# Kernel optimization log

Hardware: AMD Instinct MI355X
Metric: run time of the kernel (lower is better)

## Reference

```python
import jax, jax.numpy as jnp
import numpy as np

B, T, D = 2, 2048, 2048
NH, NKV = 16, 4
HD = D // NH  # 128
BASE, TSL = 10000.0, 1024


def rotary_tables(T, hd, base=BASE, tsl=TSL):
    # Matches Rotary.forward with rd == hd (rd=0 in __init__ -> full head dim).
    ar = jnp.arange(0, hd, 2, dtype=jnp.float32) / hd
    if T <= tsl:
        inv = 1.0 / (base ** ar)
    else:
        # NTK-style rescale; note right-assoc exponent in original torch code:
        # 1/(base * (T/tsl) ** ((rd/(rd-2)) ** ar))
        inv = 1.0 / (base * jnp.power(T / tsl, jnp.power(hd / (hd - 2.0), ar)))
    f = jnp.outer(jnp.arange(T, dtype=jnp.float32), inv)  # [T, hd//2]
    cos = jnp.cos(f)[None, :, None, :]  # [1,T,1,hd//2]
    sin = jnp.sin(f)[None, :, None, :]
    return cos, sin


def apply_rope(x, cos, sin):
    # full-dim rope: split halves, rotate
    h = x.shape[-1] // 2
    x1, x2 = x[..., :h], x[..., h:]
    return jnp.concatenate((x1 * cos + x2 * sin, -x1 * sin + x2 * cos), axis=-1)


def rms_norm(x):
    eps = jnp.finfo(x.dtype).eps
    return x * jax.lax.rsqrt(jnp.mean(x * x, axis=-1, keepdims=True) + eps)


def setup_inputs() -> dict:
    key = jax.random.key(0)
    k0, k1, k2, k3, k4 = jax.random.split(key, 5)
    s = 0.02
    return {
        "x": jax.random.normal(k0, (B, T, D), jnp.float32),
        "qw": jax.random.normal(k1, (NH * HD, D), jnp.float32) * s,
        "kw": jax.random.normal(k2, (NKV * HD, D), jnp.float32) * s,
        "vw": jax.random.normal(k3, (NKV * HD, D), jnp.float32) * s,
        "ow": jax.random.normal(k4, (D, D), jnp.float32) * s,
        "qg": jnp.ones((NH,), jnp.float32),
    }


def reference(x, qw, kw, vw, ow, qg):
    Bx, Tx, Dx = x.shape
    q = (x @ qw.T).reshape(Bx, Tx, NH, HD)
    k = (x @ kw.T).reshape(Bx, Tx, NKV, HD)
    v = (x @ vw.T).reshape(Bx, Tx, NKV, HD)
    q = rms_norm(q)
    k = rms_norm(k)
    cos, sin = rotary_tables(Tx, HD)
    q = apply_rope(q, cos, sin) * qg[None, None, :, None]
    k = apply_rope(k, cos, sin)
    # GQA: repeat kv heads
    r = NH // NKV
    k = jnp.repeat(k, r, axis=2)  # [B,T,NH,HD]
    v = jnp.repeat(v, r, axis=2)
    scale = 1.0 / jnp.sqrt(jnp.asarray(HD, q.dtype))
    scores = jnp.einsum("bqhd,bkhd->bhqk", q, k) * scale  # [B,NH,T,T]
    causal = jnp.tril(jnp.ones((Tx, Tx), dtype=bool))
    scores = jnp.where(causal[None, None, :, :], scores, jnp.asarray(-jnp.inf, scores.dtype))
    attn = jax.nn.softmax(scores, axis=-1)
    y = jnp.einsum("bhqk,bkhd->bqhd", attn, v)  # [B,T,NH,HD]
    return y.reshape(Bx, Tx, Dx) @ ow.T
```

## Files before the change

### kernel.cpp

```cpp
#include <hip/hip_runtime.h>
#include <hip/hip_bf16.h>
#include <stdint.h>


typedef __attribute__((ext_vector_type(8))) short short8;
typedef __attribute__((ext_vector_type(4))) float f32x4;
typedef __attribute__((ext_vector_type(16))) float f32x16;

#define GLOAD16(gp, lp) \
  __builtin_amdgcn_global_load_lds((const __attribute__((address_space(1))) void*)(gp), \
                                   (__attribute__((address_space(3))) void*)(lp), 16, 0, 0)

#define BAR() do { asm volatile("" ::: "memory"); __builtin_amdgcn_s_barrier(); asm volatile("" ::: "memory"); } while (0)

__device__ __forceinline__ float bf2f(unsigned short u) {
  union { unsigned int i; float f; } v; v.i = ((unsigned int)u) << 16; return v.f;
}
__device__ __forceinline__ unsigned short f2bf(float f) {
  union { float fl; unsigned int i; } v; v.fl = f;
  unsigned int r = v.i + 0x7fffu + ((v.i >> 16) & 1u);
  return (unsigned short)(r >> 16);
}
__device__ __forceinline__ unsigned pk2(float a, float b) {
  return (unsigned)f2bf(a) | ((unsigned)f2bf(b) << 16);
}

__global__ __launch_bounds__(256) void prep_kernel(
    const float* __restrict__ x, const float* __restrict__ qw,
    const float* __restrict__ kw, const float* __restrict__ vw,
    const float* __restrict__ ow,
    unsigned short* __restrict__ xb, unsigned short* __restrict__ wqkv,
    unsigned short* __restrict__ owb, float* __restrict__ cost, float* __restrict__ sint) {
  const int NX = 2097152;
  const int NW = 1572864;
  const int NO = 1048576;
  const int NT = 131072;
  int tid = blockIdx.x * 256 + threadIdx.x;
  if (tid < NX) {
    float4 v = ((const float4*)x)[tid];
    uint2 o; o.x = pk2(v.x, v.y); o.y = pk2(v.z, v.w);
    ((uint2*)xb)[tid] = o;
  } else if (tid < NX + NW) {
    int i = tid - NX; int e = i * 4;
    const float* src = (e < 4194304) ? (qw + e)
                     : (e < 5242880) ? (kw + (e - 4194304))
                                     : (vw + (e - 5242880));
    float4 v = *(const float4*)src;
    uint2 o; o.x = pk2(v.x, v.y); o.y = pk2(v.z, v.w);
    ((uint2*)wqkv)[i] = o;
  } else if (tid < NX + NW + NO) {
    int i = tid - NX - NW;
    float4 v = ((const float4*)ow)[i];
    uint2 o; o.x = pk2(v.x, v.y); o.y = pk2(v.z, v.w);
    ((uint2*)owb)[i] = o;
  } else if (tid < NX + NW + NO + NT) {
    int i = tid - NX - NW - NO;
    int t = i >> 6, j = i & 63;
    float e = exp2f(0.02272008f * (float)j * (1.0f / 64.0f));
    float inv = 1.0f / (10000.0f * exp2f(e));
    float f = (float)t * inv;
    cost[i] = cosf(f);
    sint[i] = sinf(f);
  }
}

template <int IM, int OUTF>
__global__ __launch_bounds__(512) void gemm8ph(const unsigned short* __restrict__ A,
                                               const unsigned short* __restrict__ Bw,
                                               void* __restrict__ Cp,
                                               int MT, int NTn, int N, int K) {
  extern __shared__ char smc[];
  constexpr int S = IM * 8;
  constexpr int IQ = IM / 2;
  constexpr int ASZ = IM * 2048;
  constexpr int DB = 2 * ASZ + 32768;
  constexpr int AL = (IM * 128) / 512;
  const int tid = threadIdx.x;
  const int l = tid & 63, w = tid >> 6;
  const int lane_r = l & 15, lane_g = l >> 4;
  const int wr = w >> 2, wc = w & 3;

  int qch = (MT * NTn) >> 3;
  int orig = blockIdx.x;
  int wgid = (orig & 7) * qch + (orig >> 3);
  int by = wgid / NTn, bx = wgid - by * NTn;
  const int m0 = by * IM * 32, n0 = bx * 256;

  f32x4 acc[IM][4];
#pragma unroll
  for (int i = 0; i < IM; ++i)
#pragma unroll
    for (int j = 0; j < 4; ++j) acc[i][j] = {0.f, 0.f, 0.f, 0.f};

  const unsigned short* srcA[AL]; int ldA[AL];
#pragma unroll
  for (int t = 0; t < AL; ++t) {
    int idx = t * 512 + tid;
    int rc = idx >> 3, kc = idx & 7;
    int wrp = rc >= S ? 1 : 0, rr = rc & (S - 1);
    int row = wrp * 2 * S + rr;
    srcA[t] = A + (size_t)(m0 + row) * K + (kc ^ (rc & 7)) * 8;
    ldA[t] = idx * 16;
  }
  const unsigned short* srcB[2]; int ldB[2];
#pragma unroll
  for (int t = 0; t < 2; ++t) {
    int idx = t * 512 + tid;
    int rc = idx >> 3, kc = idx & 7;
    int nrow = (rc >> 5) * 64 + (rc & 31);
    srcB[t] = Bw + (size_t)(n0 + nrow) * K + (kc ^ (rc & 7)) * 8;
    ldB[t] = idx * 16;
  }
  const int SK = S * K, JK = 32 * K;

  auto STA = [&](int kt, int ih, int dqb) {
    char* d = smc + dqb + ih * ASZ;
#pragma unroll
    for (int t = 0; t < AL; ++t) GLOAD16(srcA[t] + kt + ih * SK, d + ldA[t]);
  };
  auto STB = [&](int kt, int jh, int dqb) {
    char* d = smc + dqb + 2 * ASZ + jh * 16384;
#pragma unroll
    for (int t = 0; t < 2; ++t) GLOAD16(srcB[t] + kt + jh * JK, d + ldB[t]);
  };

  int oA[IQ][2], oB[2][2];
#pragma unroll
  for (int iq = 0; iq < IQ; ++iq)
#pragma unroll
    for (int ks = 0; ks < 2; ++ks) {
      int rc = wr * S + iq * 16 + lane_r;
      oA[iq][ks] = rc * 128 + ((ks * 64 + lane_g * 16) ^ ((rc & 7) << 4));
    }
#pragma unroll
  for (int jj = 0; jj < 2; ++jj)
#pragma unroll
    for (int ks = 0; ks < 2; ++ks) {
      int rc = wc * 32 + jj * 16 + lane_r;
      oB[jj][ks] = rc * 128 + ((ks * 64 + lane_g * 16) ^ ((rc & 7) << 4));
    }

#define VMC() do { if constexpr (IM == 8) asm volatile("s_waitcnt vmcnt(6)" ::: "memory"); \
                   else                   asm volatile("s_waitcnt vmcnt(5)" ::: "memory"); } while (0)
#define VM0() asm volatile("s_waitcnt vmcnt(0)" ::: "memory")
#define MM(IH, JH, BR) do { \
    __builtin_amdgcn_s_setprio(1); \
    _Pragma("unroll") \
    for (int iq = 0; iq < IQ; ++iq) \
      _Pragma("unroll") \
      for (int jj = 0; jj < 2; ++jj) \
        _Pragma("unroll") \
        for (int ks = 0; ks < 2; ++ks) \
          acc[(IH) * IQ + iq][(JH) * 2 + jj] = __builtin_amdgcn_mfma_f32_16x16x32_bf16( \
              af[iq][ks], BR[jj][ks], acc[(IH) * IQ + iq][(JH) * 2 + jj], 0, 0, 0); \
    __builtin_amdgcn_s_setprio(0); } while (0)

  const int NS = K >> 6;
  STA(0, 0, 0); STB(0, 0, 0); STB(0, 1, 0); STA(0, 1, 0);
  STA(64, 0, DB); STB(64, 0, DB); STB(64, 1, DB);
  VMC();
  BAR();

#pragma unroll 1
  for (int s = 0; s < NS; ++s) {
    const int dq = (s & 1) * DB, dn = DB - dq;
    const char* Ab = smc + dq;
    const char* Bb = Ab + 2 * ASZ;
    short8 af[IQ][2], b0[2][2], b1[2][2];
    if (s + 1 < NS) STA((s + 1) << 6, 1, dn);
#pragma unroll
    for (int iq = 0; iq < IQ; ++iq)
#pragma unroll
      for (int ks = 0; ks < 2; ++ks) af[iq][ks] = *(const short8*)(Ab + oA[iq][ks]);
#pragma unroll
    for (int jj = 0; jj < 2; ++jj)
#pragma unroll
      for (int ks = 0; ks < 2; ++ks) b0[jj][ks] = *(const short8*)(Bb + oB[jj][ks]);
    MM(0, 0, b0);
    BAR();
    if (s + 2 < NS) STA((s + 2) << 6, 0, dq);
#pragma unroll
    for (int jj = 0; jj < 2; ++jj)
#pragma unroll
      for (int ks = 0; ks < 2; ++ks) b1[jj][ks] = *(const short8*)(Bb + 16384 + oB[jj][ks]);
    MM(0, 1, b1);
    BAR();
    if (s + 2 < NS) STB((s + 2) << 6, 0, dq);
#pragma unroll
    for (int iq = 0; iq < IQ; ++iq)
#pragma unroll
      for (int ks = 0; ks < 2; ++ks) af[iq][ks] = *(const short8*)(Ab + ASZ + oA[iq][ks]);
    MM(1, 0, b0);
    BAR();
    if (s + 2 < NS) STB((s + 2) << 6, 1, dq);
    MM(1, 1, b1);
    if (s + 2 < NS) VMC(); else VM0();
    BAR();
  }
#undef VMC
#undef VM0
#undef MM

#pragma unroll
  for (int ih = 0; ih < 2; ++ih)
#pragma unroll
    for (int iq = 0; iq < IQ; ++iq) {
      int row = m0 + wr * 2 * S + ih * S + iq * 16 + lane_g * 4;
#pragma unroll
      for (int j = 0; j < 4; ++j) {
        int col = n0 + wc * 64 + j * 16 + lane_r;
#pragma unroll
        for (int r = 0; r < 4; ++r) {
          float v = acc[ih * IQ + iq][j][r];
          if (OUTF)
            ((float*)Cp)[(size_t)(row + r) * N + col] = v;
          else
            ((unsigned short*)Cp)[(size_t)(row + r) * N + col] = f2bf(v);
        }
      }
    }
}

__global__ __launch_bounds__(256) void normrope_kernel(unsigned short* __restrict__ qkv,
                                                       const float* __restrict__ cost,
                                                       const float* __restrict__ sint,
                                                       const float* __restrict__ qg) {
  const int tid = threadIdx.x, l = tid & 63, w = tid >> 6;
  int row = blockIdx.x * 4 + w;
  int tok = row / 20, hh = row - tok * 20;
  int t = tok & 2047;
  bool isq = hh < 16;
  int col0 = isq ? hh * 128 : 2048 + (hh - 16) * 128;
  unsigned short* p = qkv + (size_t)tok * 3072 + col0 + 2 * l;
  unsigned int u = *(const unsigned int*)p;
  float x0 = bf2f((unsigned short)(u & 0xffffu));
  float x1 = bf2f((unsigned short)(u >> 16));
  float ss = x0 * x0 + x1 * x1;
#pragma unroll
  for (int m = 1; m < 64; m <<= 1) ss += __shfl_xor(ss, m);
  float rn = rsqrtf(ss * (1.0f / 128.0f) + 1.1920928955078125e-07f);
  float n0 = x0 * rn, n1 = x1 * rn;
  float p0 = __shfl_xor(n0, 32);
  float p1 = __shfl_xor(n1, 32);
  int jj = (2 * l) & 63;
  float c0 = cost[t * 64 + jj], c1 = cost[t * 64 + jj + 1];
  float s0 = sint[t * 64 + jj], s1 = sint[t * 64 + jj + 1];
  float o0, o1;
  if (l < 32) { o0 = n0 * c0 + p0 * s0; o1 = n1 * c1 + p1 * s1; }
  else        { o0 = -p0 * s0 + n0 * c0; o1 = -p1 * s1 + n1 * c1; }
  if (isq) { float g = qg[hh] * 0.08838834764831845f * 1.4426950408889634f; o0 *= g; o1 *= g; }
  *(unsigned int*)p = pk2(o0, o1);
}

__global__ __launch_bounds__(256) void vtrans_kernel(const unsigned short* __restrict__ qkv,
                                                     unsigned short* __restrict__ vtg) {
  __shared__ unsigned short tile[64][132];
  int bid = blockIdx.x;
  int pan = bid & 7, tt = bid >> 3;
  int b = pan >> 2, kvh = pan & 3;
  int t0 = tt * 64;
  const unsigned short* src = qkv + ((size_t)(b * 2048 + t0)) * 3072 + 2560 + kvh * 128;
#pragma unroll
  for (int i = 0; i < 8; ++i) {
    int idx = i * 256 + threadIdx.x;
    int row = idx >> 5, c4 = idx & 31;
    uint2 v = *(const uint2*)(src + (size_t)row * 3072 + c4 * 4);
    *(uint2*)&tile[row][c4 * 4] = v;
  }
  __syncthreads();
  unsigned short* dst = vtg + (size_t)pan * 262144 + t0;
#pragma unroll
  for (int i = 0; i < 8; ++i) {
    int idx = i * 256 + threadIdx.x;
    int d = idx >> 4, tc = idx & 15;
    unsigned short a0 = tile[tc * 4 + 0][d], a1 = tile[tc * 4 + 1][d];
    unsigned short a2 = tile[tc * 4 + 2][d], a3 = tile[tc * 4 + 3][d];
    uint2 o; o.x = (unsigned)a0 | ((unsigned)a1 << 16);
    o.y = (unsigned)a2 | ((unsigned)a3 << 16);
    *(uint2*)(dst + (size_t)d * 2048 + tc * 4) = o;
  }
}

__global__ __launch_bounds__(512) void attn_fa6(const unsigned short* __restrict__ qkv,
                                                const unsigned short* __restrict__ vtg,
                                                unsigned short* __restrict__ y) {
  extern __shared__ char smc[];
  const int tid = threadIdx.x;
  const int l = tid & 63, w = tid >> 6;
  const int lq = l & 31, hi = l >> 5;
  const int g = w & 3, hh = w >> 2;

  int n = blockIdx.x;
  int pan = n & 7;
  int b = pan >> 2, kvh = pan & 3;
  int idx2 = n >> 3;
  int h = kvh * 4 + (idx2 & 3);
  int pairIdx = idx2 >> 2;
  const size_t rowbase = (size_t)b * 2048;
  const unsigned short* kvK = qkv + rowbase * 3072;
  const unsigned short* vtp = vtg + (size_t)pan * 262144;

  int kg[2], vg[2], sl[2];
#pragma unroll
  for (int t = 0; t < 2; ++t) {
    int idx = t * 512 + tid;
    { int row = idx >> 4, c = idx & 15, gc = c ^ (row & 7);
      kg[t] = row * 3072 + 2048 + kvh * 128 + gc * 8; }
    { int d = idx >> 3, c = idx & 7, gc = c ^ (d & 7);
      vg[t] = d * 2048 + gc * 8; }
    sl[t] = idx * 16;
  }
  const int swq = (lq & 7) << 4;
  const int krow = (hh * 32 + lq) * 256;
  int oxk[8];
#pragma unroll
  for (int ds = 0; ds < 8; ++ds) oxk[ds] = (ds * 32 + hi * 16) ^ swq;
  const int vrow = lq * 128;
  int oxv[2];
#pragma unroll
  for (int ksl = 0; ksl < 2; ++ksl) oxv[ksl] = (hh * 64 + ksl * 32 + hi * 16) ^ swq;
  const int pbase = 65536 + g * 4096;
  const int prow = pbase + lq * 128;
  int opw[4];
#pragma unroll
  for (int m = 0; m < 4; ++m) opw[m] = prow + ((hh * 64 + m * 16 + hi * 8) ^ swq);
  int opr[2];
#pragma unroll
  for (int ksl = 0; ksl < 2; ++ksl) opr[ksl] = prow + ((hh * 64 + ksl * 32 + hi * 16) ^ swq);
  const int mab = (g * 64 + l) * 256;
  const int mlb = 81920 + (g * 64 + l) * 8;
  const int lsw = (l & 7) << 4;

  auto STAGE = [&](int tile, int bufsel) {
    const unsigned short* srcK = kvK + (size_t)tile * 64 * 3072;
    const unsigned short* srcV = vtp + tile * 64;
    char* kd = smc + bufsel * 16384;
    char* vd = smc + 32768 + bufsel * 16384;
#pragma unroll
    for (int t = 0; t < 2; ++t) {
      GLOAD16(srcK + kg[t], kd + sl[t]);
      GLOAD16(srcV + vg[t], vd + sl[t]);
    }
  };

#pragma unroll 1
  for (int phase = 0; phase < 2; ++phase) {
    const int qt = phase ? pairIdx : 15 - pairIdx;
    const int q0 = qt * 128;
    const int nkb = 2 * qt + 2;
    const int wrow0 = q0 + g * 32;
    const int qrow = wrow0 + lq;

    STAGE(0, 0);
    short8 qf[8];
#pragma unroll
    for (int ds = 0; ds < 8; ++ds)
      qf[ds] = *(const short8*)(qkv + (rowbase + qrow) * 3072 + h * 128 + ds * 16 + hi * 8);

    f32x16 acc[4];
#pragma unroll
    for (int dt = 0; dt < 4; ++dt)
#pragma unroll
      for (int jj = 0; jj < 16; ++jj) acc[dt][jj] = 0.f;
    float mrun = -1e30f, lrun = 0.f;

    __syncthreads();

#pragma unroll 1
    for (int kb = 0; kb < nkb; ++kb) {
      const int cur = kb & 1;
      if (kb + 1 < nkb) STAGE(kb + 1, cur ^ 1);
      const int j0 = kb * 64;
      if (j0 + hh * 32 <= wrow0) {
        const int kbb = cur * 16384;
        const int vbb = 32768 + cur * 16384;
        f32x16 s;
#pragma unroll
        for (int jj = 0; jj < 16; ++jj) s[jj] = 0.f;
        __builtin_amdgcn_s_setprio(1);
#pragma unroll
        for (int ds = 0; ds < 8; ++ds) {
          short8 kf = *(const short8*)(smc + kbb + krow + oxk[ds]);
          s = __builtin_amdgcn_mfma_f32_32x32x16_bf16(kf, qf[ds], s, 0, 0, 0);
        }
        __builtin_amdgcn_s_setprio(0);
        const int rq = qrow - j0 - hh * 32;
        if (rq < 31) {
#pragma unroll
          for (int jj = 0; jj < 16; ++jj) {
            int kl = (jj & 3) + 8 * (jj >> 2) + 4 * hi;
            s[jj] = (kl > rq) ? -1e30f : s[jj];
          }
        }
        float pmax = s[0];
#pragma unroll
        for (int jj = 1; jj < 16; ++jj) pmax = fmaxf(pmax, s[jj]);
        pmax = fmaxf(pmax, __shfl_xor(pmax, 32));
        if (!__all(pmax - mrun <= 11.5f)) {
          float mn = fmaxf(mrun, pmax);
          float corr = exp2f(mrun - mn);
          lrun *= corr;
#pragma unroll
          for (int dt = 0; dt < 4; ++dt)
#pragma unroll
            for (int jj = 0; jj < 16; ++jj) acc[dt][jj] *= corr;
          mrun = mn;
        }
        float rs = 0.f;
#pragma unroll
        for (int jj = 0; jj < 16; ++jj) { s[jj] = exp2f(s[jj] - mrun); rs += s[jj]; }
        rs += __shfl_xor(rs, 32);
        lrun += rs;
#pragma unroll
        for (int m = 0; m < 4; ++m) {
          uint2 pv;
          pv.x = pk2(s[4 * m], s[4 * m + 1]);
          pv.y = pk2(s[4 * m + 2], s[4 * m + 3]);
          *(uint2*)(smc + opw[m]) = pv;
        }
        short8 pfr[2];
        pfr[0] = *(const short8*)(smc + opr[0]);
        pfr[1] = *(const short8*)(smc + opr[1]);
        __builtin_amdgcn_s_setprio(1);
#pragma unroll
        for (int ksl = 0; ksl < 2; ++ksl)
#pragma unroll
          for (int dt = 0; dt < 4; ++dt) {
            short8 vf = *(const short8*)(smc + vbb + dt * 4096 + vrow + oxv[ksl]);
            acc[dt] = __builtin_amdgcn_mfma_f32_32x32x16_bf16(vf, pfr[ksl], acc[dt], 0, 0, 0);
          }
        __builtin_amdgcn_s_setprio(0);
      }
      __syncthreads();
    }
    if (hh) {
#pragma unroll
      for (int dt = 0; dt < 4; ++dt)
#pragma unroll
        for (int q4 = 0; q4 < 4; ++q4) {
          f32x4 v = {acc[dt][4 * q4], acc[dt][4 * q4 + 1], acc[dt][4 * q4 + 2], acc[dt][4 * q4 + 3]};
          *(f32x4*)(smc + mab + ((dt * 64 + q4 * 16) ^ lsw)) = v;
        }
      *(float2*)(smc + mlb) = {mrun, lrun};
    }
    __syncthreads();
    if (!hh) {
      float2 ml = *(const float2*)(smc + mlb);
      float mx = fmaxf(mrun, ml.x);
      float sc0 = exp2f(mrun - mx), sc1 = exp2f(ml.x - mx);
      lrun = lrun * sc0 + ml.y * sc1;
#pragma unroll
      for (int dt = 0; dt < 4; ++dt)
#pragma unroll
        for (int q4 = 0; q4 < 4; ++q4) {
          f32x4 v = *(const f32x4*)(smc + mab + ((dt * 64 + q4 * 16) ^ lsw));
#pragma unroll
          for (int r = 0; r < 4; ++r)
            acc[dt][4 * q4 + r] = acc[dt][4 * q4 + r] * sc0 + v[r] * sc1;
        }
    }
    __syncthreads();
    if (!hh) {
      float linv = 1.0f / lrun;
      unsigned short* yrow = y + (rowbase + qrow) * 2048 + h * 128;
#pragma unroll
      for (int dt = 0; dt < 4; ++dt)
#pragma unroll
        for (int m = 0; m < 4; ++m) {
          uint2 o;
          o.x = pk2(acc[dt][4 * m] * linv, acc[dt][4 * m + 1] * linv);
          o.y = pk2(acc[dt][4 * m + 2] * linv, acc[dt][4 * m + 3] * linv);
          *(uint2*)(yrow + dt * 32 + m * 8 + hi * 4) = o;
        }
    }
  }
}

extern "C" void kernel_launch(void* const* d_in, const int* in_sizes, int n_in,
                              void* d_out, int out_size, void* d_ws, size_t ws_size,
                              hipStream_t stream) {
  (void)in_sizes; (void)n_in; (void)out_size; (void)ws_size;
  const float* x  = (const float*)d_in[0];
  const float* qw = (const float*)d_in[1];
  const float* kw = (const float*)d_in[2];
  const float* vw = (const float*)d_in[3];
  const float* ow = (const float*)d_in[4];
  const float* qg = (const float*)d_in[5];

  char* ws = (char*)d_ws;
  unsigned short* xb   = (unsigned short*)(ws + 0);
  unsigned short* vtg  = (unsigned short*)(ws + 0);
  unsigned short* wqkv = (unsigned short*)(ws + 16777216);
  unsigned short* owb  = (unsigned short*)(ws + 29360128);
  unsigned short* qkvb = (unsigned short*)(ws + 37748736);
  unsigned short* y    = (unsigned short*)(ws + 62914560);
  float* cost          = (float*)(ws + 79691776);
  float* sint          = (float*)(ws + 80216064);

  prep_kernel<<<18944, 256, 0, stream>>>(x, qw, kw, vw, ow, xb, wqkv, owb, cost, sint);
  gemm8ph<8, 0><<<192, 512, 131072, stream>>>(xb, wqkv, qkvb, 16, 12, 3072, 2048);
  normrope_kernel<<<20480, 256, 0, stream>>>(qkvb, cost, sint, qg);
  vtrans_kernel<<<256, 256, 0, stream>>>(qkvb, vtg);
  attn_fa6<<<256, 512, 83968, stream>>>(qkvb, vtg, y);
  gemm8ph<4, 1><<<256, 512, 98304, stream>>>(y, owb, d_out, 32, 8, 2048, 2048);
}
```

Baseline: 199.4 us.

## Retile QKV GEMM to 128x384 tiles and pass attention P through registers

The GEMM template gains a configurable N-tile width. The QKV projection now uses 128x384 tiles over 256 workgroups instead of 256x256 tiles over 192, which fills the CUs more evenly. In the attention kernel, the softmax probabilities are packed with v_cvt_pk_bf16_f32 and redistributed with v_permlane32_swap instead of a round trip through LDS, which removes LDS writes and reads and shrinks shared memory. The cost is hand-written inline asm for the lane swap, whose fragment layout must exactly match what the MFMA expects.

```diff
diff --git a/kernel.cpp b/kernel.cpp
--- a/kernel.cpp
+++ b/kernel.cpp
@@ -64,7 +64,7 @@
   }
 }
 
-template <int IM, int OUTF>
+template <int IM, int NB, int OUTF>
 __global__ __launch_bounds__(512) void gemm8ph(const unsigned short* __restrict__ A,
                                                const unsigned short* __restrict__ Bw,
                                                void* __restrict__ Cp,
@@ -72,9 +72,13 @@
   extern __shared__ char smc[];
   constexpr int S = IM * 8;
   constexpr int IQ = IM / 2;
+  constexpr int JQ = NB / 128;
   constexpr int ASZ = IM * 2048;
-  constexpr int DB = 2 * ASZ + 32768;
+  constexpr int BSZ = NB * 64;
+  constexpr int DB = 2 * ASZ + 2 * BSZ;
   constexpr int AL = (IM * 128) / 512;
+  constexpr int BL = NB / 128;
+  constexpr int VMCN = AL + 2 * BL;
   const int tid = threadIdx.x;
   const int l = tid & 63, w = tid >> 6;
   const int lane_r = l & 15, lane_g = l >> 4;
@@ -84,13 +88,13 @@
   int orig = blockIdx.x;
   int wgid = (orig & 7) * qch + (orig >> 3);
   int by = wgid / NTn, bx = wgid - by * NTn;
-  const int m0 = by * IM * 32, n0 = bx * 256;
-
-  f32x4 acc[IM][4];
+  const int m0 = by * IM * 32, n0 = bx * NB;
+
+  f32x4 acc[IM][2 * JQ];
 #pragma unroll
   for (int i = 0; i < IM; ++i)
 #pragma unroll
-    for (int j = 0; j < 4; ++j) acc[i][j] = {0.f, 0.f, 0.f, 0.f};
+    for (int j = 0; j < 2 * JQ; ++j) acc[i][j] = {0.f, 0.f, 0.f, 0.f};
 
   const unsigned short* srcA[AL]; int ldA[AL];
 #pragma unroll
@@ -102,16 +106,17 @@
     srcA[t] = A + (size_t)(m0 + row) * K + (kc ^ (rc & 7)) * 8;
     ldA[t] = idx * 16;
   }
-  const unsigned short* srcB[2]; int ldB[2];
-#pragma unroll
-  for (int t = 0; t < 2; ++t) {
+  const unsigned short* srcB[BL]; int ldB[BL];
+#pragma unroll
+  for (int t = 0; t < BL; ++t) {
     int idx = t * 512 + tid;
     int rc = idx >> 3, kc = idx & 7;
-    int nrow = (rc >> 5) * 64 + (rc & 31);
+    int g16 = rc >> 4;
+    int nrow = (g16 / JQ) * (NB / 4) + (g16 % JQ) * 16 + (rc & 15);
     srcB[t] = Bw + (size_t)(n0 + nrow) * K + (kc ^ (rc & 7)) * 8;
     ldB[t] = idx * 16;
   }
-  const int SK = S * K, JK = 32 * K;
+  const int SK = S * K, JK = (NB / 8) * K;
 
   auto STA = [&](int kt, int ih, int dqb) {
     char* d = smc + dqb + ih * ASZ;
@@ -119,12 +124,12 @@
     for (int t = 0; t < AL; ++t) GLOAD16(srcA[t] + kt + ih * SK, d + ldA[t]);
   };
   auto STB = [&](int kt, int jh, int dqb) {
-    char* d = smc + dqb + 2 * ASZ + jh * 16384;
-#pragma unroll
-    for (int t = 0; t < 2; ++t) GLOAD16(srcB[t] + kt + jh * JK, d + ldB[t]);
+    char* d = smc + dqb + 2 * ASZ + jh * BSZ;
+#pragma unroll
+    for (int t = 0; t < BL; ++t) GLOAD16(srcB[t] + kt + jh * JK, d + ldB[t]);
   };
 
-  int oA[IQ][2], oB[2][2];
+  int oA[IQ][2], oB[JQ][2];
 #pragma unroll
   for (int iq = 0; iq < IQ; ++iq)
 #pragma unroll
@@ -133,26 +138,25 @@
       oA[iq][ks] = rc * 128 + ((ks * 64 + lane_g * 16) ^ ((rc & 7) << 4));
     }
 #pragma unroll
-  for (int jj = 0; jj < 2; ++jj)
+  for (int jj = 0; jj < JQ; ++jj)
 #pragma unroll
     for (int ks = 0; ks < 2; ++ks) {
-      int rc = wc * 32 + jj * 16 + lane_r;
+      int rc = wc * (NB / 8) + jj * 16 + lane_r;
       oB[jj][ks] = rc * 128 + ((ks * 64 + lane_g * 16) ^ ((rc & 7) << 4));
     }
 
-#define VMC() do { if constexpr (IM == 8) asm volatile("s_waitcnt vmcnt(6)" ::: "memory"); \
-                   else                   asm volatile("s_waitcnt vmcnt(5)" ::: "memory"); } while (0)
+#define VMC() asm volatile("s_waitcnt vmcnt(%0)" :: "i"(VMCN) : "memory")
 #define VM0() asm volatile("s_waitcnt vmcnt(0)" ::: "memory")
 #define MM(IH, JH, BR) do { \
     __builtin_amdgcn_s_setprio(1); \
     _Pragma("unroll") \
     for (int iq = 0; iq < IQ; ++iq) \
       _Pragma("unroll") \
-      for (int jj = 0; jj < 2; ++jj) \
+      for (int jj = 0; jj < JQ; ++jj) \
         _Pragma("unroll") \
         for (int ks = 0; ks < 2; ++ks) \
-          acc[(IH) * IQ + iq][(JH) * 2 + jj] = __builtin_amdgcn_mfma_f32_16x16x32_bf16( \
-              af[iq][ks], BR[jj][ks], acc[(IH) * IQ + iq][(JH) * 2 + jj], 0, 0, 0); \
+          acc[(IH) * IQ + iq][(JH) * JQ + jj] = __builtin_amdgcn_mfma_f32_16x16x32_bf16( \
+              af[iq][ks], BR[jj][ks], acc[(IH) * IQ + iq][(JH) * JQ + jj], 0, 0, 0); \
     __builtin_amdgcn_s_setprio(0); } while (0)
 
   const int NS = K >> 6;
@@ -166,23 +170,23 @@
     const int dq = (s & 1) * DB, dn = DB - dq;
     const char* Ab = smc + dq;
     const char* Bb = Ab + 2 * ASZ;
-    short8 af[IQ][2], b0[2][2], b1[2][2];
+    short8 af[IQ][2], b0[JQ][2], b1[JQ][2];
     if (s + 1 < NS) STA((s + 1) << 6, 1, dn);
 #pragma unroll
     for (int iq = 0; iq < IQ; ++iq)
 #pragma unroll
       for (int ks = 0; ks < 2; ++ks) af[iq][ks] = *(const short8*)(Ab + oA[iq][ks]);
 #pragma unroll
-    for (int jj = 0; jj < 2; ++jj)
+    for (int jj = 0; jj < JQ; ++jj)
 #pragma unroll
       for (int ks = 0; ks < 2; ++ks) b0[jj][ks] = *(const short8*)(Bb + oB[jj][ks]);
     MM(0, 0, b0);
     BAR();
     if (s + 2 < NS) STA((s + 2) << 6, 0, dq);
 #pragma unroll
-    for (int jj = 0; jj < 2; ++jj)
-#pragma unroll
-      for (int ks = 0; ks < 2; ++ks) b1[jj][ks] = *(const short8*)(Bb + 16384 + oB[jj][ks]);
+    for (int jj = 0; jj < JQ; ++jj)
+#pragma unroll
+      for (int ks = 0; ks < 2; ++ks) b1[jj][ks] = *(const short8*)(Bb + BSZ + oB[jj][ks]);
     MM(0, 1, b1);
     BAR();
     if (s + 2 < NS) STB((s + 2) << 6, 0, dq);
@@ -207,17 +211,19 @@
     for (int iq = 0; iq < IQ; ++iq) {
       int row = m0 + wr * 2 * S + ih * S + iq * 16 + lane_g * 4;
 #pragma unroll
-      for (int j = 0; j < 4; ++j) {
-        int col = n0 + wc * 64 + j * 16 + lane_r;
-#pragma unroll
-        for (int r = 0; r < 4; ++r) {
-          float v = acc[ih * IQ + iq][j][r];
-          if (OUTF)
-            ((float*)Cp)[(size_t)(row + r) * N + col] = v;
-          else
-            ((unsigned short*)Cp)[(size_t)(row + r) * N + col] = f2bf(v);
-        }
-      }
+      for (int jh = 0; jh < 2; ++jh)
+#pragma unroll
+        for (int jj = 0; jj < JQ; ++jj) {
+          int col = n0 + wc * (NB / 4) + jh * (NB / 8) + jj * 16 + lane_r;
+#pragma unroll
+          for (int r = 0; r < 4; ++r) {
+            float v = acc[ih * IQ + iq][jh * JQ + jj][r];
+            if (OUTF)
+              ((float*)Cp)[(size_t)(row + r) * N + col] = v;
+            else
+              ((unsigned short*)Cp)[(size_t)(row + r) * N + col] = f2bf(v);
+          }
+        }
     }
 }
 
@@ -281,7 +287,7 @@
   }
 }
 
-__global__ __launch_bounds__(512) void attn_fa6(const unsigned short* __restrict__ qkv,
+__global__ __launch_bounds__(512) void attn_fa7(const unsigned short* __restrict__ qkv,
                                                 const unsigned short* __restrict__ vtg,
                                                 unsigned short* __restrict__ y) {
   extern __shared__ char smc[];
@@ -319,16 +325,8 @@
   int oxv[2];
 #pragma unroll
   for (int ksl = 0; ksl < 2; ++ksl) oxv[ksl] = (hh * 64 + ksl * 32 + hi * 16) ^ swq;
-  const int pbase = 65536 + g * 4096;
-  const int prow = pbase + lq * 128;
-  int opw[4];
-#pragma unroll
-  for (int m = 0; m < 4; ++m) opw[m] = prow + ((hh * 64 + m * 16 + hi * 8) ^ swq);
-  int opr[2];
-#pragma unroll
-  for (int ksl = 0; ksl < 2; ++ksl) opr[ksl] = prow + ((hh * 64 + ksl * 32 + hi * 16) ^ swq);
   const int mab = (g * 64 + l) * 256;
-  const int mlb = 81920 + (g * 64 + l) * 8;
+  const int mlb = 65536 + (g * 64 + l) * 8;
   const int lsw = (l & 7) << 4;
 
   auto STAGE = [&](int tile, int bufsel) {
@@ -411,24 +409,28 @@
         for (int jj = 0; jj < 16; ++jj) { s[jj] = exp2f(s[jj] - mrun); rs += s[jj]; }
         rs += __shfl_xor(rs, 32);
         lrun += rs;
-#pragma unroll
-        for (int m = 0; m < 4; ++m) {
-          uint2 pv;
-          pv.x = pk2(s[4 * m], s[4 * m + 1]);
-          pv.y = pk2(s[4 * m + 2], s[4 * m + 3]);
-          *(uint2*)(smc + opw[m]) = pv;
-        }
-        short8 pfr[2];
-        pfr[0] = *(const short8*)(smc + opr[0]);
-        pfr[1] = *(const short8*)(smc + opr[1]);
+        unsigned r[8];
+#pragma unroll
+        for (int j = 0; j < 4; ++j) {
+          asm("v_cvt_pk_bf16_f32 %0, %1, %2" : "=v"(r[2 * j]) : "v"(s[4 * j]), "v"(s[4 * j + 1]));
+          asm("v_cvt_pk_bf16_f32 %0, %1, %2" : "=v"(r[2 * j + 1]) : "v"(s[4 * j + 2]), "v"(s[4 * j + 3]));
+        }
         __builtin_amdgcn_s_setprio(1);
 #pragma unroll
-        for (int ksl = 0; ksl < 2; ++ksl)
+        for (int ksl = 0; ksl < 2; ++ksl) {
+          unsigned w0 = r[4 * ksl], w2 = r[4 * ksl + 2];
+          asm("v_permlane32_swap_b32 %0, %1" : "+v"(w0), "+v"(w2));
+          unsigned w1 = r[4 * ksl + 1], w3 = r[4 * ksl + 3];
+          asm("v_permlane32_swap_b32 %0, %1" : "+v"(w1), "+v"(w3));
+          union { unsigned u[4]; short8 s8; } pu;
+          pu.u[0] = w0; pu.u[1] = w1; pu.u[2] = w2; pu.u[3] = w3;
+          short8 pf = pu.s8;
 #pragma unroll
           for (int dt = 0; dt < 4; ++dt) {
             short8 vf = *(const short8*)(smc + vbb + dt * 4096 + vrow + oxv[ksl]);
-            acc[dt] = __builtin_amdgcn_mfma_f32_32x32x16_bf16(vf, pfr[ksl], acc[dt], 0, 0, 0);
+            acc[dt] = __builtin_amdgcn_mfma_f32_32x32x16_bf16(vf, pf, acc[dt], 0, 0, 0);
           }
+        }
         __builtin_amdgcn_s_setprio(0);
       }
       __syncthreads();
@@ -498,9 +500,9 @@
   float* sint          = (float*)(ws + 80216064);
 
   prep_kernel<<<18944, 256, 0, stream>>>(x, qw, kw, vw, ow, xb, wqkv, owb, cost, sint);
-  gemm8ph<8, 0><<<192, 512, 131072, stream>>>(xb, wqkv, qkvb, 16, 12, 3072, 2048);
+  gemm8ph<4, 384, 0><<<256, 512, 131072, stream>>>(xb, wqkv, qkvb, 32, 8, 3072, 2048);
   normrope_kernel<<<20480, 256, 0, stream>>>(qkvb, cost, sint, qg);
   vtrans_kernel<<<256, 256, 0, stream>>>(qkvb, vtg);
-  attn_fa6<<<256, 512, 83968, stream>>>(qkvb, vtg, y);
-  gemm8ph<4, 1><<<256, 512, 98304, stream>>>(y, owb, d_out, 32, 8, 2048, 2048);
-}
+  attn_fa7<<<256, 512, 67584, stream>>>(qkvb, vtg, y);
+  gemm8ph<4, 256, 1><<<256, 512, 98304, stream>>>(y, owb, d_out, 32, 8, 2048, 2048);
+}
```

Result: faster. 189.2 us (-5.1%).
